# Optimization experiments

Measured on AMD Instinct MI355X. Metric: run time of the kernel, lower is better.

Reference implementation:

```python
import jax, jax.numpy as jnp
import numpy as np

N_NODES = 100000
N_EDGES = 3200000
N_FEAT = 128
N_GRAPHS = 512


def setup_inputs() -> dict:
    key = jax.random.key(0)
    ks = jax.random.split(key, 12)
    x = jax.random.normal(ks[0], (N_NODES, N_FEAT), dtype=jnp.float32)
    edge_index = jax.random.randint(ks[1], (2, N_EDGES), 0, N_NODES, dtype=jnp.int64)
    batch = jnp.sort(jax.random.randint(ks[2], (N_NODES,), 0, N_GRAPHS, dtype=jnp.int64))
    def glorot(k, shape):
        lim = float(np.sqrt(6.0 / (shape[0] + shape[1])))
        return jax.random.uniform(k, shape, jnp.float32, -lim, lim)
    return {
        "x": x,
        "edge_index": edge_index,
        "batch": batch,
        "W1": glorot(ks[3], (N_FEAT, 32)),
        "b1": jnp.zeros((32,), jnp.float32),
        "W2": glorot(ks[4], (32, 64)),
        "b2": jnp.zeros((64,), jnp.float32),
        "fW1": glorot(ks[5], (96, 128)),
        "fb1": jnp.zeros((128,), jnp.float32),
        "fW2": glorot(ks[6], (128, 1)),
        "fb2": jnp.zeros((1,), jnp.float32),
    }


def _gcn_conv(h, W, b, src, dst, norm, n):
    # linear transform then normalized scatter-add aggregation (PyG GCNConv)
    h = h @ W                               # [N, out]
    msg = h[src] * norm[:, None]            # gather + scale, [E+N, out]
    agg = jax.ops.segment_sum(msg, dst, num_segments=n)
    return agg + b


def reference(x, edge_index, batch, W1, b1, W2, b2, fW1, fb1, fW2, fb2):
    n = x.shape[0]
    loop = jnp.arange(n, dtype=edge_index.dtype)
    src = jnp.concatenate([edge_index[0], loop])  # add self-loops
    dst = jnp.concatenate([edge_index[1], loop])
    # symmetric normalization: D^{-1/2} A_hat D^{-1/2}
    deg = jax.ops.segment_sum(jnp.ones(src.shape, x.dtype), dst, num_segments=n)
    dinv = jnp.where(deg > 0, jax.lax.rsqrt(deg), 0.0)
    norm = dinv[src] * dinv[dst]

    x1 = jax.nn.relu(_gcn_conv(x, W1, b1, src, dst, norm, n))   # [N, 32]
    x2 = jax.nn.relu(_gcn_conv(x1, W2, b2, src, dst, norm, n))  # [N, 64]
    xj = jnp.concatenate([x1, x2], axis=-1)                      # JK 'cat' -> [N, 96]

    # global_mean_pool over graphs
    sums = jax.ops.segment_sum(xj, batch, num_segments=N_GRAPHS)
    cnt = jax.ops.segment_sum(jnp.ones((n,), x.dtype), batch, num_segments=N_GRAPHS)
    pooled = sums / jnp.maximum(cnt, 1.0)[:, None]               # [G, 96]

    h = jax.nn.relu(pooled @ fW1 + fb1)
    return (h @ fW2 + fb2).reshape(-1)                           # [G]
```

## Files before the change

### kernel.cpp

```cpp
#include <hip/hip_runtime.h>
#include <stdint.h>

#define FEAT_IN 128
#define F1 32
#define F2 64
#define FJ 96
#define FH 128

#define BSH 8
#define BNODES 256
#define NBMAX 512
#define CH 8192
#define SRCBITS 17
#define SRCMASK 0x1FFFFu
#define PADMAX 768
#define PNPB 256
#define NP2 64
#define GR 64
#define XPAD 132

__device__ __forceinline__ unsigned f2bf(float f) {
    unsigned u = __float_as_uint(f);
    return (u + 0x7FFFu + ((u >> 16) & 1u)) >> 16;
}
__device__ __forceinline__ float bf2f(unsigned h) { return __uint_as_float(h << 16); }
__device__ __forceinline__ void bfacc8(float* a, uint4 v) {
    a[0] += bf2f(v.x & 0xffffu); a[1] += bf2f(v.x >> 16);
    a[2] += bf2f(v.y & 0xffffu); a[3] += bf2f(v.y >> 16);
    a[4] += bf2f(v.z & 0xffffu); a[5] += bf2f(v.z >> 16);
    a[6] += bf2f(v.w & 0xffffu); a[7] += bf2f(v.w >> 16);
}
__device__ __forceinline__ void fma4(float* acc, float s, float4 wv) {
    acc[0] = fmaf(s, wv.x, acc[0]);
    acc[1] = fmaf(s, wv.y, acc[1]);
    acc[2] = fmaf(s, wv.z, acc[2]);
    acc[3] = fmaf(s, wv.w, acc[3]);
}

__global__ void histA(const int* __restrict__ dst, int* __restrict__ bcnt, int nE, int nB) {
    __shared__ int h[NBMAX];
    for (int t = threadIdx.x; t < nB; t += blockDim.x) h[t] = 0;
    __syncthreads();
    int stride = gridDim.x * blockDim.x;
    for (int e = blockIdx.x * blockDim.x + threadIdx.x; e < nE; e += stride)
        atomicAdd(&h[dst[e] >> BSH], 1);
    __syncthreads();
    for (int t = threadIdx.x; t < nB; t += blockDim.x)
        if (h[t]) atomicAdd(&bcnt[t], h[t]);
}

__global__ void scanBk(const int* __restrict__ bcnt, int* __restrict__ boff,
                       int* __restrict__ bcur, int nB, int nE) {
    __shared__ int ps[256];
    int t = threadIdx.x;
    int c[4]; int s = 0;
#pragma unroll
    for (int k = 0; k < 4; ++k) { int b = t * 4 + k; c[k] = (b < nB) ? bcnt[b] : 0; s += c[k]; }
    ps[t] = s; __syncthreads();
    for (int off = 1; off < 256; off <<= 1) {
        int v = (t >= off) ? ps[t - off] : 0; __syncthreads();
        ps[t] += v; __syncthreads();
    }
    int excl = ps[t] - s;
#pragma unroll
    for (int k = 0; k < 4; ++k) {
        int b = t * 4 + k;
        if (b < nB) { boff[b] = excl; bcur[b] = excl; excl += c[k]; }
    }
    if (t == 255) boff[nB] = nE;
}

__global__ void scatterEB(const int* __restrict__ src, const int* __restrict__ dst,
                          int* __restrict__ bcur, unsigned* __restrict__ EB, int nE, int nB) {
    __shared__ int h[NBMAX], loff[NBMAX], gbase[NBMAX], lcur[NBMAX];
    __shared__ int ps[256];
    __shared__ uint2 stage[CH];
    int t = threadIdx.x;
    int e0 = blockIdx.x * CH;
    int ecnt = min(CH, nE - e0);
    if (ecnt <= 0) return;
    for (int i = t; i < nB; i += 256) h[i] = 0;
    __syncthreads();
    for (int i = t; i < ecnt; i += 256) atomicAdd(&h[dst[e0 + i] >> BSH], 1);
    __syncthreads();
    int b0 = 2 * t, b1 = 2 * t + 1;
    int c0 = (b0 < nB) ? h[b0] : 0;
    int c1 = (b1 < nB) ? h[b1] : 0;
    ps[t] = c0 + c1; __syncthreads();
    for (int off = 1; off < 256; off <<= 1) {
        int v = (t >= off) ? ps[t - off] : 0; __syncthreads();
        ps[t] += v; __syncthreads();
    }
    int excl = ps[t] - (c0 + c1);
    if (b0 < nB) { loff[b0] = excl;      lcur[b0] = excl; }
    if (b1 < nB) { loff[b1] = excl + c0; lcur[b1] = excl + c0; }
    __syncthreads();
    for (int i = t; i < nB; i += 256)
        if (h[i]) gbase[i] = atomicAdd(&bcur[i], h[i]);
    __syncthreads();
    for (int i = t; i < ecnt; i += 256) {
        int d = dst[e0 + i], s = src[e0 + i];
        int b = d >> BSH;
        int p = atomicAdd(&lcur[b], 1);
        stage[p] = make_uint2((unsigned)s, (unsigned)d);
    }
    __syncthreads();
    for (int i = t; i < ecnt; i += 256) {
        uint2 v = stage[i];
        int bb = (int)(v.y >> BSH);
        EB[gbase[bb] + (i - loff[bb])] = v.x | ((v.y & (BNODES - 1)) << SRCBITS);
    }
}

__global__ void __launch_bounds__(256)
bucketSortK(const unsigned* __restrict__ EB, const int* __restrict__ boff,
            int* __restrict__ rowptr, int* __restrict__ rowend, int* __restrict__ csrP,
            float* __restrict__ dinv, float* __restrict__ rs, int nN, int nB) {
    __shared__ int hist[BNODES];
    __shared__ int cur[BNODES];
    __shared__ int ps[256];
    int b = blockIdx.x, t = threadIdx.x;
    int beg = boff[b], end = boff[b + 1];
    hist[t] = 0;
    __syncthreads();
    for (int i = beg + t; i < end; i += 256) atomicAdd(&hist[EB[i] >> SRCBITS], 1);
    __syncthreads();
    int deg = hist[t];
    int pdeg = (deg + 3) & ~3;
    ps[t] = pdeg; __syncthreads();
    for (int off = 1; off < 256; off <<= 1) {
        int v = (t >= off) ? ps[t - off] : 0; __syncthreads();
        ps[t] += v; __syncthreads();
    }
    int base = ((beg + 3) & ~3) + b * PADMAX;
    int excl = base + ps[t] - pdeg;
    int node = (b << BSH) + t;
    if (node < nN) {
        rowptr[node] = excl;
        rowend[node] = excl + pdeg;
        dinv[node] = rsqrtf((float)deg + 1.0f);
        rs[node] = sqrtf((float)deg + 1.0f);
    }
    cur[t] = excl;
    __syncthreads();
    for (int i = beg + t; i < end; i += 256) {
        unsigned v = EB[i];
        int p = atomicAdd(&cur[v >> SRCBITS], 1);
        csrP[p] = (int)(v & SRCMASK);
    }
    __syncthreads();
    for (int p = cur[t]; p < excl + pdeg; ++p) csrP[p] = nN;
}

__global__ void __launch_bounds__(256)
gemm1v3(const float4* __restrict__ x4, const float* __restrict__ W1,
        const float* __restrict__ dinv, unsigned* __restrict__ Gc, int nN) {
    __shared__ float Ws[FEAT_IN * F1];
    __shared__ float xs[GR * XPAD];
    int t = threadIdx.x;
    for (int i = t; i < FEAT_IN * F1; i += 256) Ws[i] = W1[i];
    int rb = blockIdx.x * GR;
    for (int i = t; i < GR * 32; i += 256) {
        int r = i >> 5, c = i & 31;
        int row = rb + r;
        float4 v = (row < nN) ? x4[(size_t)row * 32 + c] : make_float4(0.f, 0.f, 0.f, 0.f);
        *(float4*)(xs + r * XPAD + c * 4) = v;
    }
    __syncthreads();
    int cg = t & 7, rg = t >> 3;
    int r0 = rg * 2, r1 = r0 + 1;
    int j0 = cg * 4;
    float acc0[4] = {0.f, 0.f, 0.f, 0.f};
    float acc1[4] = {0.f, 0.f, 0.f, 0.f};
    const float4* xa4 = (const float4*)(xs + r0 * XPAD);
    const float4* xb4 = (const float4*)(xs + r1 * XPAD);
    const float4* W4 = (const float4*)Ws;
#pragma unroll 4
    for (int kc = 0; kc < 32; ++kc) {
        float4 xa = xa4[kc];
        float4 xb = xb4[kc];
        float4 w0 = W4[(4 * kc + 0) * 8 + cg];
        float4 w1 = W4[(4 * kc + 1) * 8 + cg];
        float4 w2 = W4[(4 * kc + 2) * 8 + cg];
        float4 w3 = W4[(4 * kc + 3) * 8 + cg];
        fma4(acc0, xa.x, w0); fma4(acc0, xa.y, w1);
        fma4(acc0, xa.z, w2); fma4(acc0, xa.w, w3);
        fma4(acc1, xb.x, w0); fma4(acc1, xb.y, w1);
        fma4(acc1, xb.z, w2); fma4(acc1, xb.w, w3);
    }
    int c = j0 >> 4;
    int w = (j0 & 15) >> 1;
    int row0 = rb + r0, row1 = rb + r1;
    if (row0 < nN) {
        float dv = dinv[row0];
        uint2 val;
        val.x = f2bf(acc0[0] * dv) | (f2bf(acc0[1] * dv) << 16);
        val.y = f2bf(acc0[2] * dv) | (f2bf(acc0[3] * dv) << 16);
        *(uint2*)(Gc + ((size_t)c * (nN + 1) + row0) * 8 + w) = val;
    }
    if (row1 < nN) {
        float dv = dinv[row1];
        uint2 val;
        val.x = f2bf(acc1[0] * dv) | (f2bf(acc1[1] * dv) << 16);
        val.y = f2bf(acc1[2] * dv) | (f2bf(acc1[3] * dv) << 16);
        *(uint2*)(Gc + ((size_t)c * (nN + 1) + row1) * 8 + w) = val;
    }
}

__global__ void __launch_bounds__(256)
agg1v2(const int* __restrict__ rowptr, const int* __restrict__ rowend,
       const int* __restrict__ csrP, const unsigned* __restrict__ Gc,
       const float* __restrict__ dinv, const float* __restrict__ b1,
       unsigned* __restrict__ Hc, int nN, int K) {
    int b = blockIdx.x;
    int xcd = b & 7;
    int c = xcd & 1;
    int k = (b >> 3) * 4 + (xcd >> 1);
    if (k >= K) return;
    int t = threadIdx.x, wv = t >> 6, lane = t & 63;
    int node = k * 16 + wv * 4 + (lane >> 4);
    int slot = (lane >> 1) & 7, comp = lane & 1;
    bool vn = node < nN;
    const uint4* Gch = (const uint4*)(Gc + (size_t)c * (nN + 1) * 8);
    float a[8] = {0, 0, 0, 0, 0, 0, 0, 0};
    if (vn) {
        if ((lane & 14) == 0) bfacc8(a, Gch[(size_t)node * 2 + comp]);
        int beg = rowptr[node], endp = rowend[node];
        for (int e = beg + slot * 4; e < endp; e += 32) {
            int4 idx = *(const int4*)(csrP + e);
            uint4 r0 = Gch[(size_t)idx.x * 2 + comp];
            uint4 r1 = Gch[(size_t)idx.y * 2 + comp];
            uint4 r2 = Gch[(size_t)idx.z * 2 + comp];
            uint4 r3 = Gch[(size_t)idx.w * 2 + comp];
            bfacc8(a, r0); bfacc8(a, r1); bfacc8(a, r2); bfacc8(a, r3);
        }
    }
#pragma unroll
    for (int m = 2; m < 16; m <<= 1) {
#pragma unroll
        for (int i = 0; i < 8; ++i) a[i] += __shfl_xor(a[i], m);
    }
    if (vn && (lane & 14) == 0) {
        float dv = dinv[node];
        const float* bb = b1 + c * 16 + comp * 8;
        float h[8];
#pragma unroll
        for (int i = 0; i < 8; ++i) {
            float x1 = fmaxf(fmaf(dv, a[i], bb[i]), 0.f);
            h[i] = dv * x1;
        }
        uint4 hp;
        hp.x = f2bf(h[0]) | (f2bf(h[1]) << 16);
        hp.y = f2bf(h[2]) | (f2bf(h[3]) << 16);
        hp.z = f2bf(h[4]) | (f2bf(h[5]) << 16);
        hp.w = f2bf(h[6]) | (f2bf(h[7]) << 16);
        ((uint4*)(Hc + (size_t)c * (nN + 1) * 8))[(size_t)node * 2 + comp] = hp;
    }
}

__global__ void __launch_bounds__(256)
agg2v2(const int* __restrict__ rowptr, const int* __restrict__ rowend,
       const int* __restrict__ csrP, const unsigned* __restrict__ Hc,
       const float* __restrict__ dinv, float* __restrict__ A2, int nN, int K) {
    int b = blockIdx.x;
    int xcd = b & 7;
    int c = xcd & 1;
    int k = (b >> 3) * 4 + (xcd >> 1);
    if (k >= K) return;
    int t = threadIdx.x, wv = t >> 6, lane = t & 63;
    int node = k * 16 + wv * 4 + (lane >> 4);
    int slot = (lane >> 1) & 7, comp = lane & 1;
    bool vn = node < nN;
    const uint4* Hch = (const uint4*)(Hc + (size_t)c * (nN + 1) * 8);
    float a[8] = {0, 0, 0, 0, 0, 0, 0, 0};
    if (vn) {
        if ((lane & 14) == 0) bfacc8(a, Hch[(size_t)node * 2 + comp]);
        int beg = rowptr[node], endp = rowend[node];
        for (int e = beg + slot * 4; e < endp; e += 32) {
            int4 idx = *(const int4*)(csrP + e);
            uint4 r0 = Hch[(size_t)idx.x * 2 + comp];
            uint4 r1 = Hch[(size_t)idx.y * 2 + comp];
            uint4 r2 = Hch[(size_t)idx.z * 2 + comp];
            uint4 r3 = Hch[(size_t)idx.w * 2 + comp];
            bfacc8(a, r0); bfacc8(a, r1); bfacc8(a, r2); bfacc8(a, r3);
        }
    }
#pragma unroll
    for (int m = 2; m < 16; m <<= 1) {
#pragma unroll
        for (int i = 0; i < 8; ++i) a[i] += __shfl_xor(a[i], m);
    }
    if (vn && (lane & 14) == 0) {
        float dv = dinv[node];
        float* dst = A2 + (size_t)node * F1 + c * 16 + comp * 8;
        float4 o0 = make_float4(dv * a[0], dv * a[1], dv * a[2], dv * a[3]);
        float4 o1 = make_float4(dv * a[4], dv * a[5], dv * a[6], dv * a[7]);
        ((float4*)dst)[0] = o0;
        ((float4*)dst)[1] = o1;
    }
}

__global__ void __launch_bounds__(256)
poolX1(const unsigned* __restrict__ Hc, const float* __restrict__ rs,
       const int* __restrict__ batch, float* __restrict__ psum, int nN) {
    int t = threadIdx.x, wv = t >> 6, lane = t & 63;
    int c = wv >> 1, half = wv & 1;
    int base = blockIdx.x * PNPB + half * (PNPB / 2);
    int w32 = lane & 7, noff = lane >> 3;
    const unsigned* Hch = Hc + (size_t)c * (nN + 1) * 8;
    int feat = c * 16 + w32 * 2;
    float a0 = 0.f, a1 = 0.f;
    int curG = -1;
#pragma unroll 4
    for (int i = 0; i < PNPB / 16; ++i) {
        int node = base + noff + 8 * i;
        if (node >= nN) break;
        int bg = batch[node];
        if (bg != curG) {
            if (curG >= 0) {
                atomicAdd(&psum[(size_t)curG * FJ + feat + 0], a0);
                atomicAdd(&psum[(size_t)curG * FJ + feat + 1], a1);
            }
            a0 = a1 = 0.f; curG = bg;
        }
        unsigned v = Hch[(size_t)node * 8 + w32];
        float r = rs[node];
        a0 = fmaf(bf2f(v & 0xffffu), r, a0);
        a1 = fmaf(bf2f(v >> 16), r, a1);
    }
    if (curG >= 0) {
        atomicAdd(&psum[(size_t)curG * FJ + feat + 0], a0);
        atomicAdd(&psum[(size_t)curG * FJ + feat + 1], a1);
    }
}

__global__ void __launch_bounds__(256)
poolX2(const float* __restrict__ A2, const float* __restrict__ W2,
       const float* __restrict__ b2, const int* __restrict__ batch,
       float* __restrict__ psum, int nN) {
    __shared__ float W2s[F1 * F2];
    __shared__ float aL[NP2][F1];
    int t = threadIdx.x;
    for (int i = t; i < F1 * F2; i += 256) W2s[i] = W2[i];
    int nbase = blockIdx.x * NP2;
    {
        const float4* A4 = (const float4*)(A2 + (size_t)nbase * F1);
        float4* aL4 = (float4*)aL;
        int total4 = NP2 * F1 / 4;
        for (int i = t; i < total4; i += 256) {
            int gnode = nbase + (i >> 3);
            aL4[i] = (gnode < nN) ? A4[i] : make_float4(0.f, 0.f, 0.f, 0.f);
        }
    }
    __syncthreads();
    int wv = t >> 6, lane = t & 63;
    int n0 = wv * (NP2 / 4);
    float bj = b2[lane];
    float acc = 0.f;
    int curG = -1;
    for (int i = 0; i < NP2 / 4; ++i) {
        int node = nbase + n0 + i;
        if (node >= nN) break;
        int bg = batch[node];
        if (bg != curG) {
            if (curG >= 0) atomicAdd(&psum[(size_t)curG * FJ + F1 + lane], acc);
            acc = 0.f; curG = bg;
        }
        const float* a = aL[n0 + i];
        float dot = 0.f;
#pragma unroll
        for (int k = 0; k < F1; ++k) dot = fmaf(a[k], W2s[k * F2 + lane], dot);
        acc += fmaxf(dot + bj, 0.f);
    }
    if (curG >= 0) atomicAdd(&psum[(size_t)curG * FJ + F1 + lane], acc);
}

__global__ void cntBS(const int* __restrict__ batch, float* __restrict__ cnt,
                      int nN, int nG) {
    int g = blockIdx.x * blockDim.x + threadIdx.x;
    if (g >= nG) return;
    int lo = 0, hi = nN;
    while (lo < hi) { int m = (lo + hi) >> 1; if (batch[m] < g) lo = m + 1; else hi = m; }
    int s = lo;
    lo = 0; hi = nN;
    while (lo < hi) { int m = (lo + hi) >> 1; if (batch[m] < g + 1) lo = m + 1; else hi = m; }
    cnt[g] = (float)(lo - s);
}

__global__ void mlp_kernel(const float* __restrict__ psum, const float* __restrict__ cnt,
                           const float* __restrict__ fW1, const float* __restrict__ fb1,
                           const float* __restrict__ fW2, const float* __restrict__ fb2,
                           float* __restrict__ out) {
    __shared__ float p[FJ];
    __shared__ float red[FH];
    int g = blockIdx.x, tid = threadIdx.x;
    float c = fmaxf(cnt[g], 1.0f);
    if (tid < FJ) p[tid] = psum[g * FJ + tid] / c;
    __syncthreads();
    float acc = fb1[tid];
    for (int k = 0; k < FJ; ++k) acc = fmaf(p[k], fW1[k * FH + tid], acc);
    float h = fmaxf(acc, 0.f);
    red[tid] = h * fW2[tid];
    __syncthreads();
    for (int s = FH / 2; s > 0; s >>= 1) {
        if (tid < s) red[tid] += red[tid + s];
        __syncthreads();
    }
    if (tid == 0) out[g] = red[0] + fb2[0];
}

extern "C" void kernel_launch(void* const* d_in, const int* in_sizes, int n_in,
                              void* d_out, int out_size, void* d_ws, size_t ws_size,
                              hipStream_t stream) {
    const float* x   = (const float*)d_in[0];
    const int*   ei  = (const int*)d_in[1];
    const int*   bat = (const int*)d_in[2];
    const float* W1  = (const float*)d_in[3];
    const float* b1  = (const float*)d_in[4];
    const float* W2  = (const float*)d_in[5];
    const float* b2  = (const float*)d_in[6];
    const float* fW1 = (const float*)d_in[7];
    const float* fb1 = (const float*)d_in[8];
    const float* fW2 = (const float*)d_in[9];
    const float* fb2 = (const float*)d_in[10];
    float* out = (float*)d_out;

    int nN = in_sizes[0] / FEAT_IN;
    int nE = in_sizes[1] / 2;
    int nG = out_size;
    const int* src = ei;
    const int* dst = ei + nE;

    int nB  = (nN + BNODES - 1) >> BSH;
    int nCh = (nE + CH - 1) / CH;
    int K   = (nN + 15) / 16;
    int gridC = ((K + 3) / 4) * 8;

    char* w = (char*)d_ws;
    auto alloc = [&](size_t bytes) { char* p = w; w += (bytes + 15) & ~(size_t)15; return p; };
    int*      bcnt   = (int*)alloc(NBMAX * 4);
    int*      boff   = (int*)alloc((NBMAX + 1) * 4);
    int*      bcur   = (int*)alloc(NBMAX * 4);
    unsigned* EB     = (unsigned*)alloc((size_t)nE * 4);
    int*      rowptr = (int*)alloc((size_t)nN * 4);
    int*      rowend = (int*)alloc((size_t)nN * 4);
    int*      csrP   = (int*)alloc(((size_t)nE + (size_t)NBMAX * PADMAX + 64) * 4);
    float*    dinv   = (float*)alloc((size_t)nN * 4);
    float*    rsb    = (float*)alloc((size_t)nN * 4);
    unsigned* Gc     = (unsigned*)alloc((size_t)2 * (nN + 1) * 16 * 2);
    unsigned* Hc     = (unsigned*)alloc((size_t)2 * (nN + 1) * 16 * 2);
    float*    A2     = (float*)alloc((size_t)(nN + NP2) * F1 * 4);
    float*    psum   = (float*)alloc((size_t)nG * FJ * 4);
    float*    cnt    = (float*)alloc((size_t)nG * 4);

    hipMemsetAsync(bcnt, 0, NBMAX * 4, stream);
    hipMemsetAsync(psum, 0, (size_t)nG * FJ * 4, stream);
    for (int c = 0; c < 2; ++c) {
        hipMemsetAsync(Gc + ((size_t)c * (nN + 1) + nN) * 16, 0, 32, stream);
        hipMemsetAsync(Hc + ((size_t)c * (nN + 1) + nN) * 16, 0, 32, stream);
    }

    histA<<<1024, 256, 0, stream>>>(dst, bcnt, nE, nB);
    scanBk<<<1, 256, 0, stream>>>(bcnt, boff, bcur, nB, nE);
    scatterEB<<<nCh, 256, 0, stream>>>(src, dst, bcur, EB, nE, nB);
    bucketSortK<<<nB, 256, 0, stream>>>(EB, boff, rowptr, rowend, csrP, dinv, rsb, nN, nB);

    gemm1v3<<<(nN + GR - 1) / GR, 256, 0, stream>>>((const float4*)x, W1, dinv, Gc, nN);
    agg1v2<<<gridC, 256, 0, stream>>>(rowptr, rowend, csrP, Gc, dinv, b1, Hc, nN, K);
    agg2v2<<<gridC, 256, 0, stream>>>(rowptr, rowend, csrP, Hc, dinv, A2, nN, K);

    poolX1<<<(nN + PNPB - 1) / PNPB, 256, 0, stream>>>(Hc, rsb, bat, psum, nN);
    poolX2<<<(nN + NP2 - 1) / NP2, 256, 0, stream>>>(A2, W2, b2, bat, psum, nN);
    cntBS<<<(nG + 255) / 256, 256, 0, stream>>>(bat, cnt, nN, nG);
    mlp_kernel<<<nG, FH, 0, stream>>>(psum, cnt, fW1, fb1, fW2, fb2, out);
}
```

Baseline: 280.5 us.

## Make edge bucketing deterministic with per-chunk histograms and a global offset scan

Replaces the global-atomic bucket histogram and atomic base reservation with per-chunk histograms stored transposed, followed by a single-block scan that computes every chunk's base offset per bucket. The scatter kernel then reads its precomputed bases, packs staged entries into 32-bit words with a 16-bit bucket id, and uses smaller chunks so more blocks run. bucketSortK moves to 512 threads per block. The intent is to cut global atomic contention and shared-memory staging size. The cost is a single-block serial scan over roughly 800 chunks per bucket, which may become a latency bottleneck.

```diff
diff --git a/kernel.cpp b/kernel.cpp
--- a/kernel.cpp
+++ b/kernel.cpp
@@ -10,7 +10,7 @@
 #define BSH 8
 #define BNODES 256
 #define NBMAX 512
-#define CH 8192
+#define CH 4096
 #define SRCBITS 17
 #define SRCMASK 0x1FFFFu
 #define PADMAX 768
@@ -37,82 +37,105 @@
     acc[3] = fmaf(s, wv.w, acc[3]);
 }
 
-__global__ void histA(const int* __restrict__ dst, int* __restrict__ bcnt, int nE, int nB) {
+__global__ void histPB(const int* __restrict__ dst, int* __restrict__ gHistT,
+                       int nE, int nB, int nChP) {
     __shared__ int h[NBMAX];
-    for (int t = threadIdx.x; t < nB; t += blockDim.x) h[t] = 0;
-    __syncthreads();
-    int stride = gridDim.x * blockDim.x;
-    for (int e = blockIdx.x * blockDim.x + threadIdx.x; e < nE; e += stride)
-        atomicAdd(&h[dst[e] >> BSH], 1);
-    __syncthreads();
-    for (int t = threadIdx.x; t < nB; t += blockDim.x)
-        if (h[t]) atomicAdd(&bcnt[t], h[t]);
-}
-
-__global__ void scanBk(const int* __restrict__ bcnt, int* __restrict__ boff,
-                       int* __restrict__ bcur, int nB, int nE) {
-    __shared__ int ps[256];
-    int t = threadIdx.x;
-    int c[4]; int s = 0;
-#pragma unroll
-    for (int k = 0; k < 4; ++k) { int b = t * 4 + k; c[k] = (b < nB) ? bcnt[b] : 0; s += c[k]; }
-    ps[t] = s; __syncthreads();
-    for (int off = 1; off < 256; off <<= 1) {
-        int v = (t >= off) ? ps[t - off] : 0; __syncthreads();
-        ps[t] += v; __syncthreads();
-    }
-    int excl = ps[t] - s;
-#pragma unroll
-    for (int k = 0; k < 4; ++k) {
-        int b = t * 4 + k;
-        if (b < nB) { boff[b] = excl; bcur[b] = excl; excl += c[k]; }
-    }
-    if (t == 255) boff[nB] = nE;
-}
-
-__global__ void scatterEB(const int* __restrict__ src, const int* __restrict__ dst,
-                          int* __restrict__ bcur, unsigned* __restrict__ EB, int nE, int nB) {
-    __shared__ int h[NBMAX], loff[NBMAX], gbase[NBMAX], lcur[NBMAX];
-    __shared__ int ps[256];
-    __shared__ uint2 stage[CH];
-    int t = threadIdx.x;
-    int e0 = blockIdx.x * CH;
+    int ck = blockIdx.x, t = threadIdx.x;
+    int e0 = ck * CH;
     int ecnt = min(CH, nE - e0);
     if (ecnt <= 0) return;
     for (int i = t; i < nB; i += 256) h[i] = 0;
     __syncthreads();
     for (int i = t; i < ecnt; i += 256) atomicAdd(&h[dst[e0 + i] >> BSH], 1);
     __syncthreads();
+    for (int b = t; b < nB; b += 256) gHistT[(size_t)b * nChP + ck] = h[b];
+}
+
+__global__ void __launch_bounds__(512)
+scanAll(const int* __restrict__ gHistT, int* __restrict__ gBaseT,
+        int* __restrict__ boff, int nB, int nChP, int nE) {
+    __shared__ int tot[512];
+    __shared__ int ps[512];
+    int t = threadIdx.x;
+    int run = 0;
+    if (t < nB) {
+        const int4* hp = (const int4*)(gHistT + (size_t)t * nChP);
+        int4* gp = (int4*)(gBaseT + (size_t)t * nChP);
+        for (int q = 0; q < nChP / 4; ++q) {
+            int4 v = hp[q];
+            int4 o;
+            o.x = run; run += v.x;
+            o.y = run; run += v.y;
+            o.z = run; run += v.z;
+            o.w = run; run += v.w;
+            gp[q] = o;
+        }
+    }
+    tot[t] = (t < nB) ? run : 0;
+    __syncthreads();
+    ps[t] = tot[t]; __syncthreads();
+    for (int off = 1; off < 512; off <<= 1) {
+        int v = (t >= off) ? ps[t - off] : 0; __syncthreads();
+        ps[t] += v; __syncthreads();
+    }
+    int excl = ps[t] - tot[t];
+    if (t < nB) boff[t] = excl;
+    if (t == nB - 1) boff[nB] = excl + tot[t];
+    __syncthreads();
+    if (t < nB) {
+        int base = excl;
+        int4* gp = (int4*)(gBaseT + (size_t)t * nChP);
+        for (int q = 0; q < nChP / 4; ++q) {
+            int4 o = gp[q];
+            o.x += base; o.y += base; o.z += base; o.w += base;
+            gp[q] = o;
+        }
+    }
+}
+
+__global__ void __launch_bounds__(256)
+scatterEB2(const int* __restrict__ src, const int* __restrict__ dst,
+           const int* __restrict__ gBaseT, unsigned* __restrict__ EB,
+           int nE, int nB, int nChP) {
+    __shared__ int lh[NBMAX], loff[NBMAX], lcur[NBMAX], gbaseL[NBMAX];
+    __shared__ int ps[256];
+    __shared__ unsigned stagePack[CH];
+    __shared__ unsigned short stageBkt[CH];
+    int ck = blockIdx.x, t = threadIdx.x;
+    int e0 = ck * CH;
+    int ecnt = min(CH, nE - e0);
+    if (ecnt <= 0) return;
+    for (int i = t; i < nB; i += 256) lh[i] = 0;
+    __syncthreads();
+    for (int i = t; i < ecnt; i += 256) atomicAdd(&lh[dst[e0 + i] >> BSH], 1);
+    __syncthreads();
     int b0 = 2 * t, b1 = 2 * t + 1;
-    int c0 = (b0 < nB) ? h[b0] : 0;
-    int c1 = (b1 < nB) ? h[b1] : 0;
+    int c0 = (b0 < nB) ? lh[b0] : 0;
+    int c1 = (b1 < nB) ? lh[b1] : 0;
     ps[t] = c0 + c1; __syncthreads();
     for (int off = 1; off < 256; off <<= 1) {
         int v = (t >= off) ? ps[t - off] : 0; __syncthreads();
         ps[t] += v; __syncthreads();
     }
     int excl = ps[t] - (c0 + c1);
-    if (b0 < nB) { loff[b0] = excl;      lcur[b0] = excl; }
-    if (b1 < nB) { loff[b1] = excl + c0; lcur[b1] = excl + c0; }
-    __syncthreads();
-    for (int i = t; i < nB; i += 256)
-        if (h[i]) gbase[i] = atomicAdd(&bcur[i], h[i]);
+    if (b0 < nB) { loff[b0] = excl;      lcur[b0] = excl;      gbaseL[b0] = gBaseT[(size_t)b0 * nChP + ck]; }
+    if (b1 < nB) { loff[b1] = excl + c0; lcur[b1] = excl + c0; gbaseL[b1] = gBaseT[(size_t)b1 * nChP + ck]; }
     __syncthreads();
     for (int i = t; i < ecnt; i += 256) {
         int d = dst[e0 + i], s = src[e0 + i];
-        int b = d >> BSH;
-        int p = atomicAdd(&lcur[b], 1);
-        stage[p] = make_uint2((unsigned)s, (unsigned)d);
+        int bkt = d >> BSH;
+        int p = atomicAdd(&lcur[bkt], 1);
+        stagePack[p] = (unsigned)s | ((unsigned)(d & (BNODES - 1)) << SRCBITS);
+        stageBkt[p] = (unsigned short)bkt;
     }
     __syncthreads();
     for (int i = t; i < ecnt; i += 256) {
-        uint2 v = stage[i];
-        int bb = (int)(v.y >> BSH);
-        EB[gbase[bb] + (i - loff[bb])] = v.x | ((v.y & (BNODES - 1)) << SRCBITS);
-    }
-}
-
-__global__ void __launch_bounds__(256)
+        int bb = stageBkt[i];
+        EB[gbaseL[bb] + (i - loff[bb])] = stagePack[i];
+    }
+}
+
+__global__ void __launch_bounds__(512)
 bucketSortK(const unsigned* __restrict__ EB, const int* __restrict__ boff,
             int* __restrict__ rowptr, int* __restrict__ rowend, int* __restrict__ csrP,
             float* __restrict__ dinv, float* __restrict__ rs, int nN, int nB) {
@@ -121,35 +144,42 @@
     __shared__ int ps[256];
     int b = blockIdx.x, t = threadIdx.x;
     int beg = boff[b], end = boff[b + 1];
-    hist[t] = 0;
-    __syncthreads();
-    for (int i = beg + t; i < end; i += 256) atomicAdd(&hist[EB[i] >> SRCBITS], 1);
-    __syncthreads();
-    int deg = hist[t];
+    if (t < 256) hist[t] = 0;
+    __syncthreads();
+    for (int i = beg + t; i < end; i += 512) atomicAdd(&hist[EB[i] >> SRCBITS], 1);
+    __syncthreads();
+    int deg = (t < 256) ? hist[t] : 0;
     int pdeg = (deg + 3) & ~3;
-    ps[t] = pdeg; __syncthreads();
+    if (t < 256) ps[t] = pdeg;
+    __syncthreads();
     for (int off = 1; off < 256; off <<= 1) {
-        int v = (t >= off) ? ps[t - off] : 0; __syncthreads();
-        ps[t] += v; __syncthreads();
+        int v = (t >= off && t < 256) ? ps[t - off] : 0; __syncthreads();
+        if (t < 256) ps[t] += v;
+        __syncthreads();
     }
     int base = ((beg + 3) & ~3) + b * PADMAX;
-    int excl = base + ps[t] - pdeg;
-    int node = (b << BSH) + t;
-    if (node < nN) {
-        rowptr[node] = excl;
-        rowend[node] = excl + pdeg;
-        dinv[node] = rsqrtf((float)deg + 1.0f);
-        rs[node] = sqrtf((float)deg + 1.0f);
-    }
-    cur[t] = excl;
-    __syncthreads();
-    for (int i = beg + t; i < end; i += 256) {
+    int excl = 0;
+    if (t < 256) {
+        excl = base + ps[t] - pdeg;
+        int node = (b << BSH) + t;
+        if (node < nN) {
+            rowptr[node] = excl;
+            rowend[node] = excl + pdeg;
+            dinv[node] = rsqrtf((float)deg + 1.0f);
+            rs[node] = sqrtf((float)deg + 1.0f);
+        }
+        cur[t] = excl;
+    }
+    __syncthreads();
+    for (int i = beg + t; i < end; i += 512) {
         unsigned v = EB[i];
         int p = atomicAdd(&cur[v >> SRCBITS], 1);
         csrP[p] = (int)(v & SRCMASK);
     }
     __syncthreads();
-    for (int p = cur[t]; p < excl + pdeg; ++p) csrP[p] = nN;
+    if (t < 256) {
+        for (int p = cur[t]; p < excl + pdeg; ++p) csrP[p] = nN;
+    }
 }
 
 __global__ void __launch_bounds__(256)
@@ -431,16 +461,17 @@
     const int* src = ei;
     const int* dst = ei + nE;
 
-    int nB  = (nN + BNODES - 1) >> BSH;
-    int nCh = (nE + CH - 1) / CH;
-    int K   = (nN + 15) / 16;
+    int nB   = (nN + BNODES - 1) >> BSH;
+    int nCh  = (nE + CH - 1) / CH;
+    int nChP = (nCh + 3) & ~3;
+    int K    = (nN + 15) / 16;
     int gridC = ((K + 3) / 4) * 8;
 
     char* w = (char*)d_ws;
     auto alloc = [&](size_t bytes) { char* p = w; w += (bytes + 15) & ~(size_t)15; return p; };
-    int*      bcnt   = (int*)alloc(NBMAX * 4);
+    int*      gHistT = (int*)alloc((size_t)NBMAX * nChP * 4);
+    int*      gBaseT = (int*)alloc((size_t)NBMAX * nChP * 4);
     int*      boff   = (int*)alloc((NBMAX + 1) * 4);
-    int*      bcur   = (int*)alloc(NBMAX * 4);
     unsigned* EB     = (unsigned*)alloc((size_t)nE * 4);
     int*      rowptr = (int*)alloc((size_t)nN * 4);
     int*      rowend = (int*)alloc((size_t)nN * 4);
@@ -453,17 +484,17 @@
     float*    psum   = (float*)alloc((size_t)nG * FJ * 4);
     float*    cnt    = (float*)alloc((size_t)nG * 4);
 
-    hipMemsetAsync(bcnt, 0, NBMAX * 4, stream);
+    hipMemsetAsync(gHistT, 0, (size_t)nB * nChP * 4, stream);
     hipMemsetAsync(psum, 0, (size_t)nG * FJ * 4, stream);
     for (int c = 0; c < 2; ++c) {
         hipMemsetAsync(Gc + ((size_t)c * (nN + 1) + nN) * 16, 0, 32, stream);
         hipMemsetAsync(Hc + ((size_t)c * (nN + 1) + nN) * 16, 0, 32, stream);
     }
 
-    histA<<<1024, 256, 0, stream>>>(dst, bcnt, nE, nB);
-    scanBk<<<1, 256, 0, stream>>>(bcnt, boff, bcur, nB, nE);
-    scatterEB<<<nCh, 256, 0, stream>>>(src, dst, bcur, EB, nE, nB);
-    bucketSortK<<<nB, 256, 0, stream>>>(EB, boff, rowptr, rowend, csrP, dinv, rsb, nN, nB);
+    histPB<<<nCh, 256, 0, stream>>>(dst, gHistT, nE, nB, nChP);
+    scanAll<<<1, 512, 0, stream>>>(gHistT, gBaseT, boff, nB, nChP, nE);
+    scatterEB2<<<nCh, 256, 0, stream>>>(src, dst, gBaseT, EB, nE, nB, nChP);
+    bucketSortK<<<nB, 512, 0, stream>>>(EB, boff, rowptr, rowend, csrP, dinv, rsb, nN, nB);
 
     gemm1v3<<<(nN + GR - 1) / GR, 256, 0, stream>>>((const float4*)x, W1, dinv, Gc, nN);
     agg1v2<<<gridC, 256, 0, stream>>>(rowptr, rowend, csrP, Gc, dinv, b1, Hc, nN, K);
```

New measurement: 467.6 us. +66.7%, slower.
